# Kernel optimization log

Hardware: AMD Instinct MI355X
Metric: run time of the kernel (lower is better)

The kernel has to match this reference:

```python
import jax, jax.numpy as jnp
import numpy as np

T, C, H, W, CI = 4, 64, 96, 96, 16
PS, WS, STR0 = 7, 21, 4
KS, KA = 100, 100
SCALE = 10.0


def conv1x1(x, w, b):
    # x: [T,C,H,W], w: [O,C]
    return jnp.einsum('tchw,oc->tohw', x, w) + b[None, :, None, None]


def unfold_clip(x, ps):
    # clipped-boundary unfold: [T,C,H,W] -> [T, H*W, C*ps*ps]
    t, c, h, w = x.shape
    d = jnp.arange(ps)
    ii = jnp.clip(jnp.arange(h)[:, None] + d[None, :], 0, h - 1)  # [H,ps]
    jj = jnp.clip(jnp.arange(w)[:, None] + d[None, :], 0, w - 1)  # [W,ps]
    p = x[:, :, ii]            # [T,C,H,ps,W]
    p = p[:, :, :, :, jj]      # [T,C,H,ps,W,ps]
    p = jnp.transpose(p, (0, 2, 4, 1, 3, 5))  # [T,H,W,C,ps,ps]
    return p.reshape(t, h * w, c * ps * ps)


def setup_inputs() -> dict:
    key = jax.random.key(0)
    ks = jax.random.split(key, 9)
    s = lambda fan: 1.0 / np.sqrt(fan)
    return {
        'vid': jax.random.normal(ks[0], (T, C, H, W), jnp.float32),
        'g_w': jax.random.normal(ks[1], (CI, C), jnp.float32) * s(C),
        'g_b': jax.random.normal(ks[2], (CI,), jnp.float32) * 0.01,
        'theta_w': jax.random.normal(ks[3], (CI, C), jnp.float32) * s(C),
        'theta_b': jax.random.normal(ks[4], (CI,), jnp.float32) * 0.01,
        'phi_w': jax.random.normal(ks[5], (CI, C), jnp.float32) * s(C),
        'phi_b': jax.random.normal(ks[6], (CI,), jnp.float32) * 0.01,
        'W_w': jax.random.normal(ks[7], (C, CI), jnp.float32) * s(CI),
        'W_b': jax.random.normal(ks[8], (C,), jnp.float32) * 0.01,
    }


def reference(vid, g_w, g_b, theta_w, theta_b, phi_w, phi_b, W_w, W_b):
    t, c, h, w = vid.shape
    b1 = conv1x1(vid, g_w, g_b)          # query features  (g)
    b2 = conv1x1(vid, theta_w, theta_b)  # value features  (theta)
    b3 = conv1x1(vid, phi_w, phi_b)      # key features    (phi)

    b1u = unfold_clip(b1, PS)  # [T,HW,D]
    b2u = unfold_clip(b2, PS)
    b3u = unfold_clip(b3, PS)

    # query grid (stride0)
    qi, qj = jnp.meshgrid(jnp.arange(0, h, STR0), jnp.arange(0, w, STR0), indexing='ij')
    qi, qj = qi.reshape(-1), qj.reshape(-1)
    nq = qi.shape[0]
    qflat = qi * w + qj
    b1q = b1u[:, qflat]  # [T,nq,D]

    # centered spatial search window (stride1=1), clipped bounds
    off = jnp.arange(WS) - WS // 2
    ci = jnp.clip(qi[:, None] + off[None, :], 0, h - 1)  # [nq,WS]
    cj = jnp.clip(qj[:, None] + off[None, :], 0, w - 1)
    cand = (ci[:, :, None] * w + cj[:, None, :]).reshape(nq, WS * WS)

    # patch inner-product dists, one window offset at a time (memory-lean)
    def score(cidx):  # cidx: [nq]
        return jnp.einsum('tqd,tqd->tq', b1q, b3u[:, cidx])
    dists = jax.lax.map(score, cand.T)           # [WS*WS,T,nq]
    dists = jnp.transpose(dists, (1, 2, 0))      # [T,nq,WS*WS]

    vals, idx = jax.lax.top_k(dists, KS)
    vals, idx = vals[..., :KA], idx[..., :KA]
    yi = jax.nn.softmax(vals * SCALE, axis=-1)   # [T,nq,KA]

    pos = jnp.take_along_axis(jnp.broadcast_to(cand[None], (t,) + cand.shape), idx, axis=-1)
    patches = b2u[jnp.arange(t)[:, None, None], pos]   # [T,nq,KA,D]
    zi = jnp.einsum('tqk,tqkd->tqd', yi, patches)      # [T,nq,D]

    # fold: overlap-add scatter + counts normalization
    zi = zi.reshape(t, nq, CI, PS, PS).transpose(0, 2, 1, 3, 4).reshape(t, CI, nq * PS * PS)
    d = jnp.arange(PS)
    pi = jnp.clip(qi[:, None] + d[None, :], 0, h - 1)
    pj = jnp.clip(qj[:, None] + d[None, :], 0, w - 1)
    pix = (pi[:, :, None] * w + pj[:, None, :]).reshape(-1)
    acc = jnp.zeros((t, CI, h * w), vid.dtype).at[:, :, pix].add(zi)
    Z = jnp.zeros((h * w,), vid.dtype).at[pix].add(1.0)
    y = (acc / Z).reshape(t, CI, h, w)

    return vid + conv1x1(y, W_w, W_b)
```

## Files before the change

kernel.cpp:

```cpp
#include <hip/hip_runtime.h>
#include <hip/hip_bf16.h>
#include <hip/hip_fp16.h>
#include <math.h>

typedef __hip_bfloat16 bf16;
typedef unsigned int u32;
typedef __attribute__((ext_vector_type(8))) short short8;
typedef __attribute__((ext_vector_type(4))) float float4v;

#define T_   4
#define C_   64
#define H_   96
#define W_   96
#define CI_  16
#define HW_  9216
#define NC_  441
#define K_   100
#define HSEL 0x07060302u
#define LSEL 0x05040100u

__device__ __forceinline__ float ldbf(const void* p, int i) { return __bfloat162float(((const bf16*)p)[i]); }
__device__ __forceinline__ float ldf (const void* p, int i) { return ((const float*)p)[i]; }

__device__ __forceinline__ unsigned short f2bf(float x) {
    union { float f; u32 u; } a; a.f = x;
    u32 r = a.u + 0x7FFF + ((a.u >> 16) & 1);
    return (unsigned short)(r >> 16);
}
__device__ __forceinline__ float bf2f(unsigned short s) {
    union { u32 u; float f; } a; a.u = ((u32)s) << 16;
    return a.f;
}
__device__ __forceinline__ u32 packbf(float x) {
    unsigned short h = f2bf(x);
    unsigned short l = f2bf(x - bf2f(h));
    return ((u32)h << 16) | (u32)l;
}
__device__ __forceinline__ u32 okey(float f) {
    u32 u = __float_as_uint(f);
    return u ^ ((u & 0x80000000u) ? 0xFFFFFFFFu : 0x80000000u);
}
__device__ __forceinline__ float unokey(u32 k) {
    u32 u = (k & 0x80000000u) ? (k ^ 0x80000000u) : ~k;
    return __uint_as_float(u);
}
__device__ __forceinline__ int cntdim(int x) {
    int c = 0;
#pragma unroll
    for (int pp = 0; pp < 7; pp++) {
        int q = x - pp;
        c += (q >= 0 && q <= 92 && ((q & 3) == 0)) ? 1 : 0;
    }
    if (x == 95) c += 3;
    return c;
}

__device__ __forceinline__ int detect_flag(const void* vid, int tid, int* sflag) {
    if (tid < 64) {
        unsigned short w = ((const unsigned short*)vid)[tid * 2];
        int e = (w >> 7) & 0xFF;
        int sane = ((e >= 100 && e <= 140) || ((w & 0x7FFF) == 0)) ? 1 : 0;
#pragma unroll
        for (int off = 1; off < 64; off <<= 1) sane += __shfl_xor(sane, off);
        if (tid == 0) *sflag = (sane >= 48) ? 1 : 0;
    }
    __syncthreads();
    return *sflag;
}

__global__ __launch_bounds__(256) void conv3_k(const void* vid, const void* gw, const void* gb,
                                               const void* tw, const void* tb, const void* pw,
                                               const void* pb,
                                               u32* __restrict__ B1p, __half* __restrict__ B2h,
                                               u32* __restrict__ B3p, float* __restrict__ ACCb)
{
    __shared__ float w[3120];
    __shared__ int sflag;
    int tid = threadIdx.x;
    int isbf = detect_flag(vid, tid, &sflag);
    if (isbf) {
        for (int i = tid; i < 3120; i += 256) {
            float v;
            if (i < 1024) v = ldbf(gw, i);
            else if (i < 2048) v = ldbf(tw, i - 1024);
            else if (i < 3072) v = ldbf(pw, i - 2048);
            else if (i < 3088) v = ldbf(gb, i - 3072);
            else if (i < 3104) v = ldbf(tb, i - 3088);
            else v = ldbf(pb, i - 3104);
            w[i] = v;
        }
    } else {
        for (int i = tid; i < 3120; i += 256) {
            float v;
            if (i < 1024) v = ldf(gw, i);
            else if (i < 2048) v = ldf(tw, i - 1024);
            else if (i < 3072) v = ldf(pw, i - 2048);
            else if (i < 3088) v = ldf(gb, i - 3072);
            else if (i < 3104) v = ldf(tb, i - 3088);
            else v = ldf(pb, i - 3104);
            w[i] = v;
        }
    }
    __syncthreads();

    {
        float4v z = {0.f, 0.f, 0.f, 0.f};
        *(float4v*)(ACCb + (blockIdx.x * 256 + tid) * 4) = z;
    }

    int lane = tid & 63, og = tid >> 6;
    int g0 = blockIdx.x * 64 + lane;
    int t = g0 / HW_, pix = g0 - t * HW_;

    float a1[4], a2[4], a3[4];
#pragma unroll
    for (int k = 0; k < 4; k++) {
        a1[k] = w[3072 + og * 4 + k];
        a2[k] = w[3088 + og * 4 + k];
        a3[k] = w[3104 + og * 4 + k];
    }
    int base = t * C_ * HW_ + pix;
#pragma unroll 16
    for (int c = 0; c < C_; c++) {
        float v = isbf ? ldbf(vid, base + c * HW_) : ldf(vid, base + c * HW_);
#pragma unroll
        for (int k = 0; k < 4; k++) {
            a1[k] += v * w[(og * 4 + k) * 64 + c];
            a2[k] += v * w[1024 + (og * 4 + k) * 64 + c];
            a3[k] += v * w[2048 + (og * 4 + k) * 64 + c];
        }
    }
    int ob = g0 * 16 + og * 4;
    uint4 p1, p3;
    p1.x = packbf(a1[0]); p1.y = packbf(a1[1]); p1.z = packbf(a1[2]); p1.w = packbf(a1[3]);
    p3.x = packbf(a3[0]); p3.y = packbf(a3[1]); p3.z = packbf(a3[2]); p3.w = packbf(a3[3]);
    *(uint4*)(B1p + ob) = p1;
    *(uint4*)(B3p + ob) = p3;
    __half2 h01 = __floats2half2_rn(a2[0], a2[1]);
    __half2 h23 = __floats2half2_rn(a2[2], a2[3]);
    uint2 p2;
    p2.x = *(u32*)&h01; p2.y = *(u32*)&h23;
    *(uint2*)(B2h + ob) = p2;
}

__global__ __launch_bounds__(256, 3) void attn_k(const u32* __restrict__ B1p,
                                                 const __half* __restrict__ B2h,
                                                 const u32* __restrict__ B3p,
                                                 float* __restrict__ ACCb)
{
    __shared__ __align__(16) char SM[47248];
    short*   Win  = (short*)SM;
    float*   Sc   = (float*)(SM + 32768);
    float*   Cb   = (float*)(SM + 39824);
    int*     hist = (int*)(SM + 39824);
    float*   yiw  = (float*)(SM + 43920);
    int*     pab  = (int*)(SM + 45520);
    int*     ctl  = (int*)(SM + 47120);
    __half2* Wp   = (__half2*)SM;

    int tid = threadIdx.x;
    int tile = blockIdx.x, t = blockIdx.y;
    int qy = tile / 12, qx = tile - qy * 12;
    int qi = qy * 8, qj = qx * 8;

    const u32*    B1t = B1p + t * HW_ * 16;
    const __half* B2t = B2h + t * HW_ * 16;
    const u32*    B3t = B3p + t * HW_ * 16;

    int lane = tid & 63, wv = tid >> 6;
    int nn = lane & 15, qsel = nn >> 3, pjn = nn & 7;
    int koff = (lane >> 4) * 8;

    for (int pos = tid; pos < 1024; pos += 256) {
        int row = pos >> 5, col = pos & 31;
        int vr = min(max(qi - 10 + row, 0), 95);
        int vc = min(max(qj - 10 + col, 0), 95);
        const u32* src = B3t + (vr * 96 + vc) * 16;
        uint4 U0 = *(const uint4*)src,       U1 = *(const uint4*)(src + 4);
        uint4 U2 = *(const uint4*)(src + 8), U3 = *(const uint4*)(src + 12);
        uint4 A, B;
        A.x = __builtin_amdgcn_perm(U0.y, U0.x, HSEL);
        A.y = __builtin_amdgcn_perm(U0.w, U0.z, HSEL);
        A.z = __builtin_amdgcn_perm(U1.y, U1.x, HSEL);
        A.w = __builtin_amdgcn_perm(U1.w, U1.z, HSEL);
        B.x = __builtin_amdgcn_perm(U2.y, U2.x, HSEL);
        B.y = __builtin_amdgcn_perm(U2.w, U2.z, HSEL);
        B.z = __builtin_amdgcn_perm(U3.y, U3.x, HSEL);
        B.w = __builtin_amdgcn_perm(U3.w, U3.z, HSEL);
        *(uint4*)(Win + pos * 16)     = A;
        *(uint4*)(Win + pos * 16 + 8) = B;
    }
    __syncthreads();

#pragma unroll 1
    for (int ri = 0; ri < 2; ri++) {
        short8 Bh[4], Bl[4];
        int qiq = qi + 4 * ri, qjq = qj + 4 * qsel;
#pragma unroll
        for (int s = 0; s < 4; s++) {
            int kk0 = s * 32 + koff;
            int pi = kk0 >> 4, c0 = kk0 & 15;
            uint4 U0 = {0, 0, 0, 0}, U1 = {0, 0, 0, 0};
            if (pjn < 7 && pi < 7) {
                const u32* src = B1t + (min(qiq + pi, 95) * 96 + min(qjq + pjn, 95)) * 16 + c0;
                U0 = *(const uint4*)src;
                U1 = *(const uint4*)(src + 4);
            }
            union { uint4 u; short8 s8; } hc, lc;
            hc.u.x = __builtin_amdgcn_perm(U0.y, U0.x, HSEL);
            hc.u.y = __builtin_amdgcn_perm(U0.w, U0.z, HSEL);
            hc.u.z = __builtin_amdgcn_perm(U1.y, U1.x, HSEL);
            hc.u.w = __builtin_amdgcn_perm(U1.w, U1.z, HSEL);
            lc.u.x = __builtin_amdgcn_perm(U0.y, U0.x, LSEL);
            lc.u.y = __builtin_amdgcn_perm(U0.w, U0.z, LSEL);
            lc.u.z = __builtin_amdgcn_perm(U1.y, U1.x, LSEL);
            lc.u.w = __builtin_amdgcn_perm(U1.w, U1.z, LSEL);
            Bh[s] = hc.s8; Bl[s] = lc.s8;
        }
        float* Cw = Cb + wv * 256;
        for (int r = wv; r < 21; r += 4) {
            float psum = 0.f;
            int v = (lane >= 21) ? 1 : 0;
            int b = lane - v * 21;
#pragma unroll
            for (int st = 0; st < 2; st++) {
                float4v acc = {0.f, 0.f, 0.f, 0.f};
#pragma unroll
                for (int s = 0; s < 4; s++) {
                    int arow = 4 * ri + r + 2 * s + (lane >> 5);
                    int aoff = (arow * 32 + st * 16 + nn) * 16 + ((lane >> 4) & 1) * 8;
                    short8 A = *(const short8*)(Win + aoff);
                    acc = __builtin_amdgcn_mfma_f32_16x16x32_bf16(A, Bh[s], acc, 0, 0, 0);
                    acc = __builtin_amdgcn_mfma_f32_16x16x32_bf16(A, Bl[s], acc, 0, 0, 0);
                }
                *(float4v*)(Cw + nn * 16 + (lane >> 4) * 4) = acc;
                if (lane < 42) {
#pragma unroll
                    for (int pj = 0; pj < 7; pj++) {
                        int sp = b + 4 * v + pj;
                        if ((sp >> 4) == st) psum += Cw[(8 * v + pj) * 16 + (sp & 15)];
                    }
                }
            }
            if (lane < 42) Sc[(ri * 2 + v) * 441 + r * 21 + b] = psum;
        }
    }
    __syncthreads();

    for (int pos = tid; pos < 1024; pos += 256) {
        int row = pos >> 5, col = pos & 31;
        int vr = min(max(qi - 10 + row, 0), 95);
        int vc = min(max(qj - 10 + col, 0), 95);
        const u32* src = B3t + (vr * 96 + vc) * 16;
        uint4 U0 = *(const uint4*)src,       U1 = *(const uint4*)(src + 4);
        uint4 U2 = *(const uint4*)(src + 8), U3 = *(const uint4*)(src + 12);
        uint4 A, B;
        A.x = __builtin_amdgcn_perm(U0.y, U0.x, LSEL);
        A.y = __builtin_amdgcn_perm(U0.w, U0.z, LSEL);
        A.z = __builtin_amdgcn_perm(U1.y, U1.x, LSEL);
        A.w = __builtin_amdgcn_perm(U1.w, U1.z, LSEL);
        B.x = __builtin_amdgcn_perm(U2.y, U2.x, LSEL);
        B.y = __builtin_amdgcn_perm(U2.w, U2.z, LSEL);
        B.z = __builtin_amdgcn_perm(U3.y, U3.x, LSEL);
        B.w = __builtin_amdgcn_perm(U3.w, U3.z, LSEL);
        *(uint4*)(Win + pos * 16)     = A;
        *(uint4*)(Win + pos * 16 + 8) = B;
    }
    __syncthreads();

#pragma unroll 1
    for (int ri = 0; ri < 2; ri++) {
        short8 Bh[4];
        int qiq = qi + 4 * ri, qjq = qj + 4 * qsel;
#pragma unroll
        for (int s = 0; s < 4; s++) {
            int kk0 = s * 32 + koff;
            int pi = kk0 >> 4, c0 = kk0 & 15;
            uint4 U0 = {0, 0, 0, 0}, U1 = {0, 0, 0, 0};
            if (pjn < 7 && pi < 7) {
                const u32* src = B1t + (min(qiq + pi, 95) * 96 + min(qjq + pjn, 95)) * 16 + c0;
                U0 = *(const uint4*)src;
                U1 = *(const uint4*)(src + 4);
            }
            union { uint4 u; short8 s8; } hc;
            hc.u.x = __builtin_amdgcn_perm(U0.y, U0.x, HSEL);
            hc.u.y = __builtin_amdgcn_perm(U0.w, U0.z, HSEL);
            hc.u.z = __builtin_amdgcn_perm(U1.y, U1.x, HSEL);
            hc.u.w = __builtin_amdgcn_perm(U1.w, U1.z, HSEL);
            Bh[s] = hc.s8;
        }
        float* Cw = Cb + wv * 256;
        for (int r = wv; r < 21; r += 4) {
            float psum = 0.f;
            int v = (lane >= 21) ? 1 : 0;
            int b = lane - v * 21;
#pragma unroll
            for (int st = 0; st < 2; st++) {
                float4v acc = {0.f, 0.f, 0.f, 0.f};
#pragma unroll
                for (int s = 0; s < 4; s++) {
                    int arow = 4 * ri + r + 2 * s + (lane >> 5);
                    int aoff = (arow * 32 + st * 16 + nn) * 16 + ((lane >> 4) & 1) * 8;
                    short8 A = *(const short8*)(Win + aoff);
                    acc = __builtin_amdgcn_mfma_f32_16x16x32_bf16(A, Bh[s], acc, 0, 0, 0);
                }
                *(float4v*)(Cw + nn * 16 + (lane >> 4) * 4) = acc;
                if (lane < 42) {
#pragma unroll
                    for (int pj = 0; pj < 7; pj++) {
                        int sp = b + 4 * v + pj;
                        if ((sp >> 4) == st) psum += Cw[(8 * v + pj) * 16 + (sp & 15)];
                    }
                }
            }
            if (lane < 42) Sc[(ri * 2 + v) * 441 + r * 21 + b] += psum;
        }
    }
    __syncthreads();

    for (int idx = tid; idx < 1764; idx += 256) {
        int g = idx / 441, k = idx - g * 441;
        int a = k / 21, b = k - a * 21;
        int ri = g >> 1, ci = g & 1;
        int qiq = qi + 4 * ri, qjq = qj + 4 * ci;
        int alo = max(0, 10 - qiq), ahi = min(20, 105 - qiq);
        int blo = max(0, 10 - qjq), bhi = min(20, 105 - qjq);
        int ae = min(max(a, alo), ahi), be = min(max(b, blo), bhi);
        if (ae != a || be != b) Sc[g * 441 + k] = Sc[g * 441 + ae * 21 + be];
    }
    for (int pos = tid; pos < 992; pos += 256) {
        int row = pos >> 5, col = pos & 31;
        int vr = min(max(qi - 10 + row, 0), 95);
        int vc = min(max(qj - 10 + col, 0), 95);
        const __half* src = B2t + (vr * 96 + vc) * 16;
        *(int4*)(Wp + pos * 8)     = *(const int4*)src;
        *(int4*)(Wp + pos * 8 + 4) = *(const int4*)(src + 8);
    }
    hist[tid] = 0; hist[256 + tid] = 0; hist[512 + tid] = 0; hist[768 + tid] = 0;
    if (tid < 32) ctl[tid] = ((tid & 7) == 1) ? K_ : 0;
    __syncthreads();

    int g = wv;
    u32 kreg[7]; int ni = 0;
    u32 kmax = 0;
    for (int i = lane; i < NC_; i += 64) {
        u32 k = okey(Sc[g * 441 + i]);
        kmax = max(kmax, k);
        kreg[ni++] = k;
    }
#pragma unroll
    for (int off = 1; off < 64; off <<= 1) kmax = max(kmax, (u32)__shfl_xor((int)kmax, off));

    for (int ps = 3; ps >= 0; ps--) {
        u32 pref = (u32)ctl[g * 8];
        if (!ctl[g * 8 + 3]) {
            for (int a = 0; a < ni; a++) {
                u32 k = kreg[a];
                if (ps == 3 || (k >> ((ps + 1) * 8)) == pref)
                    atomicAdd(&hist[g * 256 + ((k >> (ps * 8)) & 255)], 1);
            }
        }
        __syncthreads();
        if (!ctl[g * 8 + 3]) {
            int4 hv = *(int4*)(hist + g * 256 + lane * 4);
            int local = hv.x + hv.y + hv.z + hv.w;
            int s = local;
#pragma unroll
            for (int off = 1; off < 64; off <<= 1) {
                int tt = __shfl_down(s, off);
                if (lane + off < 64) s += tt;
            }
            int c4 = s - local;
            int c3 = c4 + hv.w, c2 = c3 + hv.z, c1 = c2 + hv.y, c0 = s;
            int need = ctl[g * 8 + 1];
            u32 pf = (u32)ctl[g * 8];
            int cums[5] = {c0, c1, c2, c3, c4};
            int hk[4] = {hv.x, hv.y, hv.z, hv.w};
#pragma unroll
            for (int k = 0; k < 4; k++) {
                if (cums[k] >= need && cums[k + 1] < need) {
                    int newneed = need - cums[k + 1];
                    ctl[g * 8]     = (int)((pf << 8) | (u32)(lane * 4 + k));
                    ctl[g * 8 + 1] = newneed;
                    if (newneed == hk[k] || ps == 0) { ctl[g * 8 + 3] = 1; ctl[g * 8 + 2] = 8 * ps; }
                }
            }
            int4 zz = {0, 0, 0, 0};
            *(int4*)(hist + g * 256 + lane * 4) = zz;
        }
        __syncthreads();
        if (ctl[3] && ctl[11] && ctl[19] && ctl[27]) break;
    }

    int ri = g >> 1, ci = g & 1;
    int qiq = qi + 4 * ri, qjq = qj + 4 * ci;
    {
        u32 theta = (u32)ctl[g * 8];
        int shift = ctl[g * 8 + 2];
        int need  = ctl[g * 8 + 1];
        int base  = K_ - need;
        int alo = max(0, 10 - qiq), ahi = min(20, 105 - qiq);
        int blo = max(0, 10 - qjq), bhi = min(20, 105 - qjq);
        int a2 = 0;
        for (int i = lane; i < NC_; i += 64) {
            u32 k = kreg[a2++];
            u32 hp = k >> shift;
            int slot = -1;
            if (hp > theta) slot = atomicAdd(&ctl[g * 8 + 4], 1);
            else if (hp == theta) {
                int j = atomicAdd(&ctl[g * 8 + 5], 1);
                if (j < need) slot = base + j;
            }
            if (slot >= 0) {
                int a = i / 21, b = i - a * 21;
                int ae = min(max(a, alo), ahi), be = min(max(b, blo), bhi);
                yiw[g * 100 + slot] = Sc[g * 441 + i];
                pab[g * 100 + slot] = ((ae + 4 * ri) << 8) | (be + 4 * ci);
            }
        }
    }
    {
        float m = unokey(kmax);
        float wa = expf((yiw[g * 100 + lane] - m) * 10.f);
        float wb2 = (lane < 36) ? expf((yiw[g * 100 + 64 + lane] - m) * 10.f) : 0.f;
        float ssum = wa + wb2;
#pragma unroll
        for (int off = 1; off < 64; off <<= 1) ssum += __shfl_xor(ssum, off);
        float inv = 1.f / ssum;
        yiw[g * 100 + lane] = wa * inv;
        if (lane < 36) yiw[g * 100 + 64 + lane] = wb2 * inv;
    }

    if (lane < 49) {
        int pi = lane / 7, pj = lane - pi * 7;
        int rsel = lane & 1;
        __half2 z[8];
#pragma unroll
        for (int j = 0; j < 8; j++) z[j] = __float2half2_rn(0.f);
        for (int k = 0; k < K_; k++) {
            float y = yiw[g * 100 + k];
            int pp = pab[g * 100 + k];
            int row = (pp >> 8) + pi, col = (pp & 255) + pj;
            const __half2* cell = Wp + (row * 32 + col) * 8;
            int4 A0 = *(const int4*)(cell + rsel * 4);
            int4 A1 = *(const int4*)(cell + 4 - rsel * 4);
            const __half2* pa = (const __half2*)&A0;
            const __half2* pb2 = (const __half2*)&A1;
            __half2 yh = __float2half2_rn(y);
#pragma unroll
            for (int j = 0; j < 4; j++) {
                z[j]     = __hfma2(pa[j],  yh, z[j]);
                z[4 + j] = __hfma2(pb2[j], yh, z[4 + j]);
            }
        }
        int orow = min(qiq + pi, 95), ocol = min(qjq + pj, 95);
        float* dst = ACCb + t * CI_ * HW_ + orow * 96 + ocol;
        int c0 = rsel * 8, c1 = 8 - c0;
#pragma unroll
        for (int jh = 0; jh < 4; jh++) {
            atomicAdd(dst + (c0 + 2 * jh) * HW_,     __low2float(z[jh]));
            atomicAdd(dst + (c0 + 2 * jh + 1) * HW_, __high2float(z[jh]));
            atomicAdd(dst + (c1 + 2 * jh) * HW_,     __low2float(z[4 + jh]));
            atomicAdd(dst + (c1 + 2 * jh + 1) * HW_, __high2float(z[4 + jh]));
        }
    }
}

__global__ __launch_bounds__(256) void out_k(const void* vid, const void* Ww, const void* Wb,
                                             const float* __restrict__ ACCb, void* out)
{
    __shared__ float w[1088];
    __shared__ int sflag;
    int tid = threadIdx.x;
    int isbf = detect_flag(vid, tid, &sflag);
    if (isbf) { for (int i = tid; i < 1088; i += 256) w[i] = (i < 1024) ? ldbf(Ww, i) : ldbf(Wb, i - 1024); }
    else      { for (int i = tid; i < 1088; i += 256) w[i] = (i < 1024) ? ldf (Ww, i) : ldf (Wb, i - 1024); }
    __syncthreads();

    int lane5 = tid & 31, oct = tid >> 5;
    int g0 = blockIdx.x * 32 + lane5;
    int t = g0 / HW_, pix = g0 - t * HW_;
    int pi = pix / 96, pj = pix - pi * 96;
    float invz = 1.f / (float)(cntdim(pi) * cntdim(pj));

    float y[CI_];
    int ab = t * CI_ * HW_ + pix;
#pragma unroll
    for (int ci = 0; ci < CI_; ci++) y[ci] = ACCb[ab + ci * HW_] * invz;

    int vb = t * C_ * HW_ + pix;
#pragma unroll
    for (int co = oct * 8; co < oct * 8 + 8; co++) {
        float s = w[1024 + co];
#pragma unroll
        for (int ci = 0; ci < CI_; ci++) s += w[co * 16 + ci] * y[ci];
        int idx = vb + co * HW_;
        float vv = isbf ? ldbf(vid, idx) : ldf(vid, idx);
        float r = vv + s;
        if (isbf) ((bf16*)out)[idx] = __float2bfloat16(r);
        else      ((float*)out)[idx] = r;
    }
}

extern "C" void kernel_launch(void* const* d_in, const int* in_sizes, int n_in,
                              void* d_out, int out_size, void* d_ws, size_t ws_size,
                              hipStream_t stream)
{
    char* ws = (char*)d_ws;
    u32*    B1p  = (u32*)ws;
    __half* B2h  = (__half*)(ws + 2359296);
    u32*    B3p  = (u32*)(ws + 3538944);
    float*  ACCb = (float*)(ws + 5898240);

    conv3_k<<<dim3(576), dim3(256), 0, stream>>>(d_in[0], d_in[1], d_in[2], d_in[3], d_in[4],
                                                 d_in[5], d_in[6], B1p, B2h, B3p, ACCb);
    attn_k<<<dim3(144, T_), dim3(256), 0, stream>>>(B1p, B2h, B3p, ACCb);
    out_k<<<dim3(1152), dim3(256), 0, stream>>>(d_in[0], d_in[7], d_in[8], ACCb, d_out);
}
```

Measured before the change: 182.5 us.

## Make attention kernel persistent with atomic tile counter work distribution

Turns attn_k into a persistent kernel: 512 blocks repeatedly grab one of the 576 (timestep, tile) work items through a global atomic counter, which conv3_k resets. The launch-bounds occupancy hint drops from 3 to 2 blocks per CU. The aim is to balance uneven per-tile cost and cut the tail of a one-shot grid. In exchange it adds a per-tile atomic plus barrier and gives up some occupancy hint. Tiles with heavier top-k selection can also still leave a few blocks finishing late.

After: 220.4 us. 1.21x slower.

```diff
diff --git a/kernel.cpp b/kernel.cpp
--- a/kernel.cpp
+++ b/kernel.cpp
@@ -16,6 +16,7 @@
 #define HW_  9216
 #define NC_  441
 #define K_   100
+#define NTILE 576
 #define HSEL 0x07060302u
 #define LSEL 0x05040100u
 
@@ -72,11 +73,13 @@
                                                const void* tw, const void* tb, const void* pw,
                                                const void* pb,
                                                u32* __restrict__ B1p, __half* __restrict__ B2h,
-                                               u32* __restrict__ B3p, float* __restrict__ ACCb)
+                                               u32* __restrict__ B3p, float* __restrict__ ACCb,
+                                               int* __restrict__ cnt)
 {
     __shared__ float w[3120];
     __shared__ int sflag;
     int tid = threadIdx.x;
+    if (blockIdx.x == 0 && tid == 0) *cnt = 0;
     int isbf = detect_flag(vid, tid, &sflag);
     if (isbf) {
         for (int i = tid; i < 3120; i += 256) {
@@ -143,12 +146,13 @@
     *(uint2*)(B2h + ob) = p2;
 }
 
-__global__ __launch_bounds__(256, 3) void attn_k(const u32* __restrict__ B1p,
+__global__ __launch_bounds__(256, 2) void attn_k(const u32* __restrict__ B1p,
                                                  const __half* __restrict__ B2h,
                                                  const u32* __restrict__ B3p,
-                                                 float* __restrict__ ACCb)
+                                                 float* __restrict__ ACCb,
+                                                 int* __restrict__ cnt)
 {
-    __shared__ __align__(16) char SM[47248];
+    __shared__ __align__(16) char SM[47264];
     short*   Win  = (short*)SM;
     float*   Sc   = (float*)(SM + 32768);
     float*   Cb   = (float*)(SM + 39824);
@@ -156,313 +160,313 @@
     float*   yiw  = (float*)(SM + 43920);
     int*     pab  = (int*)(SM + 45520);
     int*     ctl  = (int*)(SM + 47120);
+    int*     tctl = (int*)(SM + 47248);
     __half2* Wp   = (__half2*)SM;
 
     int tid = threadIdx.x;
-    int tile = blockIdx.x, t = blockIdx.y;
-    int qy = tile / 12, qx = tile - qy * 12;
-    int qi = qy * 8, qj = qx * 8;
-
-    const u32*    B1t = B1p + t * HW_ * 16;
-    const __half* B2t = B2h + t * HW_ * 16;
-    const u32*    B3t = B3p + t * HW_ * 16;
-
     int lane = tid & 63, wv = tid >> 6;
     int nn = lane & 15, qsel = nn >> 3, pjn = nn & 7;
     int koff = (lane >> 4) * 8;
 
-    for (int pos = tid; pos < 1024; pos += 256) {
-        int row = pos >> 5, col = pos & 31;
-        int vr = min(max(qi - 10 + row, 0), 95);
-        int vc = min(max(qj - 10 + col, 0), 95);
-        const u32* src = B3t + (vr * 96 + vc) * 16;
-        uint4 U0 = *(const uint4*)src,       U1 = *(const uint4*)(src + 4);
-        uint4 U2 = *(const uint4*)(src + 8), U3 = *(const uint4*)(src + 12);
-        uint4 A, B;
-        A.x = __builtin_amdgcn_perm(U0.y, U0.x, HSEL);
-        A.y = __builtin_amdgcn_perm(U0.w, U0.z, HSEL);
-        A.z = __builtin_amdgcn_perm(U1.y, U1.x, HSEL);
-        A.w = __builtin_amdgcn_perm(U1.w, U1.z, HSEL);
-        B.x = __builtin_amdgcn_perm(U2.y, U2.x, HSEL);
-        B.y = __builtin_amdgcn_perm(U2.w, U2.z, HSEL);
-        B.z = __builtin_amdgcn_perm(U3.y, U3.x, HSEL);
-        B.w = __builtin_amdgcn_perm(U3.w, U3.z, HSEL);
-        *(uint4*)(Win + pos * 16)     = A;
-        *(uint4*)(Win + pos * 16 + 8) = B;
-    }
-    __syncthreads();
+    for (;;) {
+        if (tid == 0) tctl[0] = atomicAdd(cnt, 1);
+        __syncthreads();
+        int tileid = tctl[0];
+        if (tileid >= NTILE) break;
+        int t = tileid / 144, tile = tileid - t * 144;
+        int qy = tile / 12, qx = tile - qy * 12;
+        int qi = qy * 8, qj = qx * 8;
+
+        const u32*    B1t = B1p + t * HW_ * 16;
+        const __half* B2t = B2h + t * HW_ * 16;
+        const u32*    B3t = B3p + t * HW_ * 16;
+
+        for (int pos = tid; pos < 1024; pos += 256) {
+            int row = pos >> 5, col = pos & 31;
+            int vr = min(max(qi - 10 + row, 0), 95);
+            int vc = min(max(qj - 10 + col, 0), 95);
+            const u32* src = B3t + (vr * 96 + vc) * 16;
+            uint4 U0 = *(const uint4*)src,       U1 = *(const uint4*)(src + 4);
+            uint4 U2 = *(const uint4*)(src + 8), U3 = *(const uint4*)(src + 12);
+            uint4 A, B;
+            A.x = __builtin_amdgcn_perm(U0.y, U0.x, HSEL);
+            A.y = __builtin_amdgcn_perm(U0.w, U0.z, HSEL);
+            A.z = __builtin_amdgcn_perm(U1.y, U1.x, HSEL);
+            A.w = __builtin_amdgcn_perm(U1.w, U1.z, HSEL);
+            B.x = __builtin_amdgcn_perm(U2.y, U2.x, HSEL);
+            B.y = __builtin_amdgcn_perm(U2.w, U2.z, HSEL);
+            B.z = __builtin_amdgcn_perm(U3.y, U3.x, HSEL);
+            B.w = __builtin_amdgcn_perm(U3.w, U3.z, HSEL);
+            *(uint4*)(Win + pos * 16)     = A;
+            *(uint4*)(Win + pos * 16 + 8) = B;
+        }
+        __syncthreads();
 
 #pragma unroll 1
-    for (int ri = 0; ri < 2; ri++) {
-        short8 Bh[4], Bl[4];
-        int qiq = qi + 4 * ri, qjq = qj + 4 * qsel;
-#pragma unroll
-        for (int s = 0; s < 4; s++) {
-            int kk0 = s * 32 + koff;
-            int pi = kk0 >> 4, c0 = kk0 & 15;
-            uint4 U0 = {0, 0, 0, 0}, U1 = {0, 0, 0, 0};
-            if (pjn < 7 && pi < 7) {
-                const u32* src = B1t + (min(qiq + pi, 95) * 96 + min(qjq + pjn, 95)) * 16 + c0;
-                U0 = *(const uint4*)src;
-                U1 = *(const uint4*)(src + 4);
-            }
-            union { uint4 u; short8 s8; } hc, lc;
-            hc.u.x = __builtin_amdgcn_perm(U0.y, U0.x, HSEL);
-            hc.u.y = __builtin_amdgcn_perm(U0.w, U0.z, HSEL);
-            hc.u.z = __builtin_amdgcn_perm(U1.y, U1.x, HSEL);
-            hc.u.w = __builtin_amdgcn_perm(U1.w, U1.z, HSEL);
-            lc.u.x = __builtin_amdgcn_perm(U0.y, U0.x, LSEL);
-            lc.u.y = __builtin_amdgcn_perm(U0.w, U0.z, LSEL);
-            lc.u.z = __builtin_amdgcn_perm(U1.y, U1.x, LSEL);
-            lc.u.w = __builtin_amdgcn_perm(U1.w, U1.z, LSEL);
-            Bh[s] = hc.s8; Bl[s] = lc.s8;
-        }
-        float* Cw = Cb + wv * 256;
-        for (int r = wv; r < 21; r += 4) {
-            float psum = 0.f;
-            int v = (lane >= 21) ? 1 : 0;
-            int b = lane - v * 21;
-#pragma unroll
-            for (int st = 0; st < 2; st++) {
-                float4v acc = {0.f, 0.f, 0.f, 0.f};
-#pragma unroll
-                for (int s = 0; s < 4; s++) {
-                    int arow = 4 * ri + r + 2 * s + (lane >> 5);
-                    int aoff = (arow * 32 + st * 16 + nn) * 16 + ((lane >> 4) & 1) * 8;
-                    short8 A = *(const short8*)(Win + aoff);
-                    acc = __builtin_amdgcn_mfma_f32_16x16x32_bf16(A, Bh[s], acc, 0, 0, 0);
-                    acc = __builtin_amdgcn_mfma_f32_16x16x32_bf16(A, Bl[s], acc, 0, 0, 0);
-                }
-                *(float4v*)(Cw + nn * 16 + (lane >> 4) * 4) = acc;
-                if (lane < 42) {
-#pragma unroll
-                    for (int pj = 0; pj < 7; pj++) {
-                        int sp = b + 4 * v + pj;
-                        if ((sp >> 4) == st) psum += Cw[(8 * v + pj) * 16 + (sp & 15)];
+        for (int ri = 0; ri < 2; ri++) {
+            short8 Bh[4], Bl[4];
+            int qiq = qi + 4 * ri, qjq = qj + 4 * qsel;
+#pragma unroll
+            for (int s = 0; s < 4; s++) {
+                int kk0 = s * 32 + koff;
+                int pi = kk0 >> 4, c0 = kk0 & 15;
+                uint4 U0 = {0, 0, 0, 0}, U1 = {0, 0, 0, 0};
+                if (pjn < 7 && pi < 7) {
+                    const u32* src = B1t + (min(qiq + pi, 95) * 96 + min(qjq + pjn, 95)) * 16 + c0;
+                    U0 = *(const uint4*)src;
+                    U1 = *(const uint4*)(src + 4);
+                }
+                union { uint4 u; short8 s8; } hc, lc;
+                hc.u.x = __builtin_amdgcn_perm(U0.y, U0.x, HSEL);
+                hc.u.y = __builtin_amdgcn_perm(U0.w, U0.z, HSEL);
+                hc.u.z = __builtin_amdgcn_perm(U1.y, U1.x, HSEL);
+                hc.u.w = __builtin_amdgcn_perm(U1.w, U1.z, HSEL);
+                lc.u.x = __builtin_amdgcn_perm(U0.y, U0.x, LSEL);
+                lc.u.y = __builtin_amdgcn_perm(U0.w, U0.z, LSEL);
+                lc.u.z = __builtin_amdgcn_perm(U1.y, U1.x, LSEL);
+                lc.u.w = __builtin_amdgcn_perm(U1.w, U1.z, LSEL);
+                Bh[s] = hc.s8; Bl[s] = lc.s8;
+            }
+            float* Cw = Cb + wv * 256;
+            for (int r = wv; r < 21; r += 4) {
+                float psum = 0.f;
+                int v = (lane >= 21) ? 1 : 0;
+                int b = lane - v * 21;
+#pragma unroll
+                for (int st = 0; st < 2; st++) {
+                    float4v acc = {0.f, 0.f, 0.f, 0.f};
+#pragma unroll
+                    for (int s = 0; s < 4; s++) {
+                        int arow = 4 * ri + r + 2 * s + (lane >> 5);
+                        int aoff = (arow * 32 + st * 16 + nn) * 16 + ((lane >> 4) & 1) * 8;
+                        short8 A = *(const short8*)(Win + aoff);
+                        acc = __builtin_amdgcn_mfma_f32_16x16x32_bf16(A, Bh[s], acc, 0, 0, 0);
+                        acc = __builtin_amdgcn_mfma_f32_16x16x32_bf16(A, Bl[s], acc, 0, 0, 0);
                     }
-                }
-            }
-            if (lane < 42) Sc[(ri * 2 + v) * 441 + r * 21 + b] = psum;
-        }
-    }
-    __syncthreads();
-
-    for (int pos = tid; pos < 1024; pos += 256) {
-        int row = pos >> 5, col = pos & 31;
-        int vr = min(max(qi - 10 + row, 0), 95);
-        int vc = min(max(qj - 10 + col, 0), 95);
-        const u32* src = B3t + (vr * 96 + vc) * 16;
-        uint4 U0 = *(const uint4*)src,       U1 = *(const uint4*)(src + 4);
-        uint4 U2 = *(const uint4*)(src + 8), U3 = *(const uint4*)(src + 12);
-        uint4 A, B;
-        A.x = __builtin_amdgcn_perm(U0.y, U0.x, LSEL);
-        A.y = __builtin_amdgcn_perm(U0.w, U0.z, LSEL);
-        A.z = __builtin_amdgcn_perm(U1.y, U1.x, LSEL);
-        A.w = __builtin_amdgcn_perm(U1.w, U1.z, LSEL);
-        B.x = __builtin_amdgcn_perm(U2.y, U2.x, LSEL);
-        B.y = __builtin_amdgcn_perm(U2.w, U2.z, LSEL);
-        B.z = __builtin_amdgcn_perm(U3.y, U3.x, LSEL);
-        B.w = __builtin_amdgcn_perm(U3.w, U3.z, LSEL);
-        *(uint4*)(Win + pos * 16)     = A;
-        *(uint4*)(Win + pos * 16 + 8) = B;
-    }
-    __syncthreads();
+                    *(float4v*)(Cw + nn * 16 + (lane >> 4) * 4) = acc;
+                    if (lane < 42) {
+#pragma unroll
+                        for (int pj = 0; pj < 7; pj++) {
+                            int sp = b + 4 * v + pj;
+                            if ((sp >> 4) == st) psum += Cw[(8 * v + pj) * 16 + (sp & 15)];
+                        }
+                    }
+                }
+                if (lane < 42) Sc[(ri * 2 + v) * 441 + r * 21 + b] = psum;
+            }
+        }
+        __syncthreads();
+
+        for (int pos = tid; pos < 1024; pos += 256) {
+            int row = pos >> 5, col = pos & 31;
+            int vr = min(max(qi - 10 + row, 0), 95);
+            int vc = min(max(qj - 10 + col, 0), 95);
+            const u32* src = B3t + (vr * 96 + vc) * 16;
+            uint4 U0 = *(const uint4*)src,       U1 = *(const uint4*)(src + 4);
+            uint4 U2 = *(const uint4*)(src + 8), U3 = *(const uint4*)(src + 12);
+            uint4 A, B;
+            A.x = __builtin_amdgcn_perm(U0.y, U0.x, LSEL);
+            A.y = __builtin_amdgcn_perm(U0.w, U0.z, LSEL);
+            A.z = __builtin_amdgcn_perm(U1.y, U1.x, LSEL);
+            A.w = __builtin_amdgcn_perm(U1.w, U1.z, LSEL);
+            B.x = __builtin_amdgcn_perm(U2.y, U2.x, LSEL);
+            B.y = __builtin_amdgcn_perm(U2.w, U2.z, LSEL);
+            B.z = __builtin_amdgcn_perm(U3.y, U3.x, LSEL);
+            B.w = __builtin_amdgcn_perm(U3.w, U3.z, LSEL);
+            *(uint4*)(Win + pos * 16)     = A;
+            *(uint4*)(Win + pos * 16 + 8) = B;
+        }
+        __syncthreads();
 
 #pragma unroll 1
-    for (int ri = 0; ri < 2; ri++) {
-        short8 Bh[4];
-        int qiq = qi + 4 * ri, qjq = qj + 4 * qsel;
-#pragma unroll
-        for (int s = 0; s < 4; s++) {
-            int kk0 = s * 32 + koff;
-            int pi = kk0 >> 4, c0 = kk0 & 15;
-            uint4 U0 = {0, 0, 0, 0}, U1 = {0, 0, 0, 0};
-            if (pjn < 7 && pi < 7) {
-                const u32* src = B1t + (min(qiq + pi, 95) * 96 + min(qjq + pjn, 95)) * 16 + c0;
-                U0 = *(const uint4*)src;
-                U1 = *(const uint4*)(src + 4);
-            }
-            union { uint4 u; short8 s8; } hc;
-            hc.u.x = __builtin_amdgcn_perm(U0.y, U0.x, HSEL);
-            hc.u.y = __builtin_amdgcn_perm(U0.w, U0.z, HSEL);
-            hc.u.z = __builtin_amdgcn_perm(U1.y, U1.x, HSEL);
-            hc.u.w = __builtin_amdgcn_perm(U1.w, U1.z, HSEL);
-            Bh[s] = hc.s8;
-        }
-        float* Cw = Cb + wv * 256;
-        for (int r = wv; r < 21; r += 4) {
-            float psum = 0.f;
-            int v = (lane >= 21) ? 1 : 0;
-            int b = lane - v * 21;
-#pragma unroll
-            for (int st = 0; st < 2; st++) {
-                float4v acc = {0.f, 0.f, 0.f, 0.f};
-#pragma unroll
-                for (int s = 0; s < 4; s++) {
-                    int arow = 4 * ri + r + 2 * s + (lane >> 5);
-                    int aoff = (arow * 32 + st * 16 + nn) * 16 + ((lane >> 4) & 1) * 8;
-                    short8 A = *(const short8*)(Win + aoff);
-                    acc = __builtin_amdgcn_mfma_f32_16x16x32_bf16(A, Bh[s], acc, 0, 0, 0);
-                }
-                *(float4v*)(Cw + nn * 16 + (lane >> 4) * 4) = acc;
-                if (lane < 42) {
-#pragma unroll
-                    for (int pj = 0; pj < 7; pj++) {
-                        int sp = b + 4 * v + pj;
-                        if ((sp >> 4) == st) psum += Cw[(8 * v + pj) * 16 + (sp & 15)];
+        for (int ri = 0; ri < 2; ri++) {
+            short8 Bh[4];
+            int qiq = qi + 4 * ri, qjq = qj + 4 * qsel;
+#pragma unroll
+            for (int s = 0; s < 4; s++) {
+                int kk0 = s * 32 + koff;
+                int pi = kk0 >> 4, c0 = kk0 & 15;
+                uint4 U0 = {0, 0, 0, 0}, U1 = {0, 0, 0, 0};
+                if (pjn < 7 && pi < 7) {
+                    const u32* src = B1t + (min(qiq + pi, 95) * 96 + min(qjq + pjn, 95)) * 16 + c0;
+                    U0 = *(const uint4*)src;
+                    U1 = *(const uint4*)(src + 4);
+                }
+                union { uint4 u; short8 s8; } hc;
+                hc.u.x = __builtin_amdgcn_perm(U0.y, U0.x, HSEL);
+                hc.u.y = __builtin_amdgcn_perm(U0.w, U0.z, HSEL);
+                hc.u.z = __builtin_amdgcn_perm(U1.y, U1.x, HSEL);
+                hc.u.w = __builtin_amdgcn_perm(U1.w, U1.z, HSEL);
+                Bh[s] = hc.s8;
+            }
+            float* Cw = Cb + wv * 256;
+            for (int r = wv; r < 21; r += 4) {
+                float psum = 0.f;
+                int v = (lane >= 21) ? 1 : 0;
+                int b = lane - v * 21;
+#pragma unroll
+                for (int st = 0; st < 2; st++) {
+                    float4v acc = {0.f, 0.f, 0.f, 0.f};
+#pragma unroll
+                    for (int s = 0; s < 4; s++) {
+                        int arow = 4 * ri + r + 2 * s + (lane >> 5);
+                        int aoff = (arow * 32 + st * 16 + nn) * 16 + ((lane >> 4) & 1) * 8;
+                        short8 A = *(const short8*)(Win + aoff);
+                        acc = __builtin_amdgcn_mfma_f32_16x16x32_bf16(A, Bh[s], acc, 0, 0, 0);
                     }
-                }
-            }
-            if (lane < 42) Sc[(ri * 2 + v) * 441 + r * 21 + b] += psum;
-        }
-    }
-    __syncthreads();
-
-    for (int idx = tid; idx < 1764; idx += 256) {
-        int g = idx / 441, k = idx - g * 441;
-        int a = k / 21, b = k - a * 21;
+                    *(float4v*)(Cw + nn * 16 + (lane >> 4) * 4) = acc;
+                    if (lane < 42) {
+#pragma unroll
+                        for (int pj = 0; pj < 7; pj++) {
+                            int sp = b + 4 * v + pj;
+                            if ((sp >> 4) == st) psum += Cw[(8 * v + pj) * 16 + (sp & 15)];
+                        }
+                    }
+                }
+                if (lane < 42) Sc[(ri * 2 + v) * 441 + r * 21 + b] += psum;
+            }
+        }
+        __syncthreads();
+
+        for (int pos = tid; pos < 992; pos += 256) {
+            int row = pos >> 5, col = pos & 31;
+            int vr = min(max(qi - 10 + row, 0), 95);
+            int vc = min(max(qj - 10 + col, 0), 95);
+            const __half* src = B2t + (vr * 96 + vc) * 16;
+            *(int4*)(Wp + pos * 8)     = *(const int4*)src;
+            *(int4*)(Wp + pos * 8 + 4) = *(const int4*)(src + 8);
+        }
+        hist[tid] = 0; hist[256 + tid] = 0; hist[512 + tid] = 0; hist[768 + tid] = 0;
+        if (tid < 32) ctl[tid] = ((tid & 7) == 1) ? K_ : 0;
+        __syncthreads();
+
+        int g = wv;
         int ri = g >> 1, ci = g & 1;
         int qiq = qi + 4 * ri, qjq = qj + 4 * ci;
         int alo = max(0, 10 - qiq), ahi = min(20, 105 - qiq);
         int blo = max(0, 10 - qjq), bhi = min(20, 105 - qjq);
-        int ae = min(max(a, alo), ahi), be = min(max(b, blo), bhi);
-        if (ae != a || be != b) Sc[g * 441 + k] = Sc[g * 441 + ae * 21 + be];
-    }
-    for (int pos = tid; pos < 992; pos += 256) {
-        int row = pos >> 5, col = pos & 31;
-        int vr = min(max(qi - 10 + row, 0), 95);
-        int vc = min(max(qj - 10 + col, 0), 95);
-        const __half* src = B2t + (vr * 96 + vc) * 16;
-        *(int4*)(Wp + pos * 8)     = *(const int4*)src;
-        *(int4*)(Wp + pos * 8 + 4) = *(const int4*)(src + 8);
-    }
-    hist[tid] = 0; hist[256 + tid] = 0; hist[512 + tid] = 0; hist[768 + tid] = 0;
-    if (tid < 32) ctl[tid] = ((tid & 7) == 1) ? K_ : 0;
-    __syncthreads();
-
-    int g = wv;
-    u32 kreg[7]; int ni = 0;
-    u32 kmax = 0;
-    for (int i = lane; i < NC_; i += 64) {
-        u32 k = okey(Sc[g * 441 + i]);
-        kmax = max(kmax, k);
-        kreg[ni++] = k;
-    }
-#pragma unroll
-    for (int off = 1; off < 64; off <<= 1) kmax = max(kmax, (u32)__shfl_xor((int)kmax, off));
-
-    for (int ps = 3; ps >= 0; ps--) {
-        u32 pref = (u32)ctl[g * 8];
-        if (!ctl[g * 8 + 3]) {
-            for (int a = 0; a < ni; a++) {
-                u32 k = kreg[a];
-                if (ps == 3 || (k >> ((ps + 1) * 8)) == pref)
-                    atomicAdd(&hist[g * 256 + ((k >> (ps * 8)) & 255)], 1);
-            }
-        }
-        __syncthreads();
-        if (!ctl[g * 8 + 3]) {
-            int4 hv = *(int4*)(hist + g * 256 + lane * 4);
-            int local = hv.x + hv.y + hv.z + hv.w;
-            int s = local;
-#pragma unroll
-            for (int off = 1; off < 64; off <<= 1) {
-                int tt = __shfl_down(s, off);
-                if (lane + off < 64) s += tt;
-            }
-            int c4 = s - local;
-            int c3 = c4 + hv.w, c2 = c3 + hv.z, c1 = c2 + hv.y, c0 = s;
-            int need = ctl[g * 8 + 1];
-            u32 pf = (u32)ctl[g * 8];
-            int cums[5] = {c0, c1, c2, c3, c4};
-            int hk[4] = {hv.x, hv.y, hv.z, hv.w};
-#pragma unroll
-            for (int k = 0; k < 4; k++) {
-                if (cums[k] >= need && cums[k + 1] < need) {
-                    int newneed = need - cums[k + 1];
-                    ctl[g * 8]     = (int)((pf << 8) | (u32)(lane * 4 + k));
-                    ctl[g * 8 + 1] = newneed;
-                    if (newneed == hk[k] || ps == 0) { ctl[g * 8 + 3] = 1; ctl[g * 8 + 2] = 8 * ps; }
-                }
-            }
-            int4 zz = {0, 0, 0, 0};
-            *(int4*)(hist + g * 256 + lane * 4) = zz;
-        }
-        __syncthreads();
-        if (ctl[3] && ctl[11] && ctl[19] && ctl[27]) break;
-    }
-
-    int ri = g >> 1, ci = g & 1;
-    int qiq = qi + 4 * ri, qjq = qj + 4 * ci;
-    {
-        u32 theta = (u32)ctl[g * 8];
-        int shift = ctl[g * 8 + 2];
-        int need  = ctl[g * 8 + 1];
-        int base  = K_ - need;
-        int alo = max(0, 10 - qiq), ahi = min(20, 105 - qiq);
-        int blo = max(0, 10 - qjq), bhi = min(20, 105 - qjq);
-        int a2 = 0;
+        u32 kreg[7]; int ni = 0;
+        u32 kmax = 0;
         for (int i = lane; i < NC_; i += 64) {
-            u32 k = kreg[a2++];
-            u32 hp = k >> shift;
-            int slot = -1;
-            if (hp > theta) slot = atomicAdd(&ctl[g * 8 + 4], 1);
-            else if (hp == theta) {
-                int j = atomicAdd(&ctl[g * 8 + 5], 1);
-                if (j < need) slot = base + j;
-            }
-            if (slot >= 0) {
-                int a = i / 21, b = i - a * 21;
-                int ae = min(max(a, alo), ahi), be = min(max(b, blo), bhi);
-                yiw[g * 100 + slot] = Sc[g * 441 + i];
-                pab[g * 100 + slot] = ((ae + 4 * ri) << 8) | (be + 4 * ci);
-            }
-        }
-    }
-    {
-        float m = unokey(kmax);
-        float wa = expf((yiw[g * 100 + lane] - m) * 10.f);
-        float wb2 = (lane < 36) ? expf((yiw[g * 100 + 64 + lane] - m) * 10.f) : 0.f;
-        float ssum = wa + wb2;
-#pragma unroll
-        for (int off = 1; off < 64; off <<= 1) ssum += __shfl_xor(ssum, off);
-        float inv = 1.f / ssum;
-        yiw[g * 100 + lane] = wa * inv;
-        if (lane < 36) yiw[g * 100 + 64 + lane] = wb2 * inv;
-    }
-
-    if (lane < 49) {
-        int pi = lane / 7, pj = lane - pi * 7;
-        int rsel = lane & 1;
-        __half2 z[8];
-#pragma unroll
-        for (int j = 0; j < 8; j++) z[j] = __float2half2_rn(0.f);
-        for (int k = 0; k < K_; k++) {
-            float y = yiw[g * 100 + k];
-            int pp = pab[g * 100 + k];
-            int row = (pp >> 8) + pi, col = (pp & 255) + pj;
-            const __half2* cell = Wp + (row * 32 + col) * 8;
-            int4 A0 = *(const int4*)(cell + rsel * 4);
-            int4 A1 = *(const int4*)(cell + 4 - rsel * 4);
-            const __half2* pa = (const __half2*)&A0;
-            const __half2* pb2 = (const __half2*)&A1;
-            __half2 yh = __float2half2_rn(y);
-#pragma unroll
-            for (int j = 0; j < 4; j++) {
-                z[j]     = __hfma2(pa[j],  yh, z[j]);
-                z[4 + j] = __hfma2(pb2[j], yh, z[4 + j]);
-            }
-        }
-        int orow = min(qiq + pi, 95), ocol = min(qjq + pj, 95);
-        float* dst = ACCb + t * CI_ * HW_ + orow * 96 + ocol;
-        int c0 = rsel * 8, c1 = 8 - c0;
-#pragma unroll
-        for (int jh = 0; jh < 4; jh++) {
-            atomicAdd(dst + (c0 + 2 * jh) * HW_,     __low2float(z[jh]));
-            atomicAdd(dst + (c0 + 2 * jh + 1) * HW_, __high2float(z[jh]));
-            atomicAdd(dst + (c1 + 2 * jh) * HW_,     __low2float(z[4 + jh]));
-            atomicAdd(dst + (c1 + 2 * jh + 1) * HW_, __high2float(z[4 + jh]));
-        }
+            int aa = i / 21, bb = i - aa * 21;
+            int ae = min(max(aa, alo), ahi), be = min(max(bb, blo), bhi);
+            u32 k = okey(Sc[g * 441 + ae * 21 + be]);
+            kmax = max(kmax, k);
+            kreg[ni++] = k;
+        }
+#pragma unroll
+        for (int off = 1; off < 64; off <<= 1) kmax = max(kmax, (u32)__shfl_xor((int)kmax, off));
+
+        for (int ps = 3; ps >= 0; ps--) {
+            u32 pref = (u32)ctl[g * 8];
+            if (!ctl[g * 8 + 3]) {
+                for (int a = 0; a < ni; a++) {
+                    u32 k = kreg[a];
+                    if (ps == 3 || (k >> ((ps + 1) * 8)) == pref)
+                        atomicAdd(&hist[g * 256 + ((k >> (ps * 8)) & 255)], 1);
+                }
+            }
+            __syncthreads();
+            if (!ctl[g * 8 + 3]) {
+                int4 hv = *(int4*)(hist + g * 256 + lane * 4);
+                int local = hv.x + hv.y + hv.z + hv.w;
+                int s = local;
+#pragma unroll
+                for (int off = 1; off < 64; off <<= 1) {
+                    int tt = __shfl_down(s, off);
+                    if (lane + off < 64) s += tt;
+                }
+                int c4 = s - local;
+                int c3 = c4 + hv.w, c2 = c3 + hv.z, c1 = c2 + hv.y, c0 = s;
+                int need = ctl[g * 8 + 1];
+                u32 pf = (u32)ctl[g * 8];
+                int cums[5] = {c0, c1, c2, c3, c4};
+                int hk[4] = {hv.x, hv.y, hv.z, hv.w};
+#pragma unroll
+                for (int k = 0; k < 4; k++) {
+                    if (cums[k] >= need && cums[k + 1] < need) {
+                        int newneed = need - cums[k + 1];
+                        ctl[g * 8]     = (int)((pf << 8) | (u32)(lane * 4 + k));
+                        ctl[g * 8 + 1] = newneed;
+                        if (newneed == hk[k] || ps == 0) { ctl[g * 8 + 3] = 1; ctl[g * 8 + 2] = 8 * ps; }
+                    }
+                }
+                int4 zz = {0, 0, 0, 0};
+                *(int4*)(hist + g * 256 + lane * 4) = zz;
+            }
+            __syncthreads();
+            if (ctl[3] && ctl[11] && ctl[19] && ctl[27]) break;
+        }
+
+        {
+            u32 theta = (u32)ctl[g * 8];
+            int shift = ctl[g * 8 + 2];
+            int need  = ctl[g * 8 + 1];
+            int base  = K_ - need;
+            int a2 = 0;
+            for (int i = lane; i < NC_; i += 64) {
+                u32 k = kreg[a2++];
+                u32 hp = k >> shift;
+                int slot = -1;
+                if (hp > theta) slot = atomicAdd(&ctl[g * 8 + 4], 1);
+                else if (hp == theta) {
+                    int j = atomicAdd(&ctl[g * 8 + 5], 1);
+                    if (j < need) slot = base + j;
+                }
+                if (slot >= 0) {
+                    int a = i / 21, b = i - a * 21;
+                    int ae = min(max(a, alo), ahi), be = min(max(b, blo), bhi);
+                    yiw[g * 100 + slot] = unokey(k);
+                    pab[g * 100 + slot] = ((ae + 4 * ri) << 8) | (be + 4 * ci);
+                }
+            }
+        }
+        {
+            float m = unokey(kmax);
+            float wa = expf((yiw[g * 100 + lane] - m) * 10.f);
+            float wb2 = (lane < 36) ? expf((yiw[g * 100 + 64 + lane] - m) * 10.f) : 0.f;
+            float ssum = wa + wb2;
+#pragma unroll
+            for (int off = 1; off < 64; off <<= 1) ssum += __shfl_xor(ssum, off);
+            float inv = 1.f / ssum;
+            yiw[g * 100 + lane] = wa * inv;
+            if (lane < 36) yiw[g * 100 + 64 + lane] = wb2 * inv;
+        }
+
+        if (lane < 49) {
+            int pi = lane / 7, pj = lane - pi * 7;
+            int rsel = lane & 1;
+            __half2 z[8];
+#pragma unroll
+            for (int j = 0; j < 8; j++) z[j] = __float2half2_rn(0.f);
+            for (int k = 0; k < K_; k++) {
+                float y = yiw[g * 100 + k];
+                int pp = pab[g * 100 + k];
+                int row = (pp >> 8) + pi, col = (pp & 255) + pj;
+                const __half2* cell = Wp + (row * 32 + col) * 8;
+                int4 A0 = *(const int4*)(cell + rsel * 4);
+                int4 A1 = *(const int4*)(cell + 4 - rsel * 4);
+                const __half2* pa = (const __half2*)&A0;
+                const __half2* pb2 = (const __half2*)&A1;
+                __half2 yh = __float2half2_rn(y);
+#pragma unroll
+                for (int j = 0; j < 4; j++) {
+                    z[j]     = __hfma2(pa[j],  yh, z[j]);
+                    z[4 + j] = __hfma2(pb2[j], yh, z[4 + j]);
+                }
+            }
+            int orow = min(qiq + pi, 95), ocol = min(qjq + pj, 95);
+            float* dst = ACCb + t * CI_ * HW_ + orow * 96 + ocol;
+            int c0 = rsel * 8, c1 = 8 - c0;
+#pragma unroll
+            for (int jh = 0; jh < 4; jh++) {
+                atomicAdd(dst + (c0 + 2 * jh) * HW_,     __low2float(z[jh]));
+                atomicAdd(dst + (c0 + 2 * jh + 1) * HW_, __high2float(z[jh]));
+                atomicAdd(dst + (c1 + 2 * jh) * HW_,     __low2float(z[4 + jh]));
+                atomicAdd(dst + (c1 + 2 * jh + 1) * HW_, __high2float(z[4 + jh]));
+            }
+        }
+        __syncthreads();
     }
 }
 
@@ -511,9 +515,10 @@
     __half* B2h  = (__half*)(ws + 2359296);
     u32*    B3p  = (u32*)(ws + 3538944);
     float*  ACCb = (float*)(ws + 5898240);
+    int*    cnt  = (int*)(ws + 8257536);
 
     conv3_k<<<dim3(576), dim3(256), 0, stream>>>(d_in[0], d_in[1], d_in[2], d_in[3], d_in[4],
-                                                 d_in[5], d_in[6], B1p, B2h, B3p, ACCb);
-    attn_k<<<dim3(144, T_), dim3(256), 0, stream>>>(B1p, B2h, B3p, ACCb);
+                                                 d_in[5], d_in[6], B1p, B2h, B3p, ACCb, cnt);
+    attn_k<<<dim3(512), dim3(256), 0, stream>>>(B1p, B2h, B3p, ACCb, cnt);
     out_k<<<dim3(1152), dim3(256), 0, stream>>>(d_in[0], d_in[7], d_in[8], ACCb, d_out);
 }
```
